# Performance work log

Measured on AMD Instinct MI355X. Metric: run time of the kernel, lower is better.

Reference implementation:

```python
import jax, jax.numpy as jnp
import numpy as np

N_NODES = 20000
N_EDGES = 5000
STEPS = 50
INFECTION_RATE = 0.01
RECOVERY_RATE = 0.038
EDGE_DENSITY = 0.002  # ~10 hyperedges per node on average


def setup_inputs() -> dict:
    key = jax.random.key(0)
    k1, k2 = jax.random.split(key, 2)
    # initial SIR state per node: valid probability rows summing to 1
    u = jax.random.uniform(k1, (N_NODES, 3), dtype=jnp.float32)
    x = u / u.sum(axis=1, keepdims=True)
    # binary hypergraph incidence matrix (num_hyperedges, num_nodes)
    H = (jax.random.uniform(k2, (N_EDGES, N_NODES)) < EDGE_DENSITY).astype(jnp.float32)
    beta = jnp.full((N_NODES,), INFECTION_RATE, dtype=jnp.float32)
    gamma = jnp.full((N_NODES,), RECOVERY_RATE, dtype=jnp.float32)
    return {"x": x, "H": H, "beta": beta, "gamma": gamma, "steps": STEPS}


def reference(x, H, beta, gamma, steps):
    # x: (N, 3) [S, I, R] per node; H: (E, N) incidence.
    def step(state, _):
        S, I, R = state[:, 0], state[:, 1], state[:, 2]
        # hypergraph message passing: node -> hyperedge -> node
        new_cases = beta * (S * (H.T @ (H @ I)))
        new_recovery = gamma * I
        nxt = jnp.stack(
            [S - new_cases, I + new_cases - new_recovery, R + new_recovery], axis=1
        )
        nxt = jnp.maximum(nxt, 0.0)                       # clamp(min=0)
        nxt = nxt / nxt.sum(axis=1, keepdims=True)        # per-node row normalize
        return nxt, nxt

    _, traj = jax.lax.scan(step, x, None, length=steps - 1)
    # output[0] = initial state, then steps-1 simulated updates -> (steps, N, 3)
    return jnp.concatenate([x[None], traj], axis=0)
```

## Files before the change

kernel.cpp:

```cpp
#include <hip/hip_runtime.h>
#include <hip/hip_bf16.h>


#define EDGE_CAP 96
#define NODE_CAP 32

__global__ void zero_counts_kernel(int* edge_cnt, int* node_cnt, int n_edges, int n_nodes) {
    int i = blockIdx.x * blockDim.x + threadIdx.x;
    if (i < n_edges) edge_cnt[i] = 0;
    if (i < n_nodes) node_cnt[i] = 0;
}

__global__ void build_adjacency_kernel(const float* __restrict__ H,
                                       int* __restrict__ edge_cnt,
                                       int* __restrict__ edge_nodes,
                                       int* __restrict__ node_cnt,
                                       int* __restrict__ node_edges,
                                       int n_nodes) {
    const int e = blockIdx.x;
    const float* row = H + (size_t)e * n_nodes;
    const int n4 = n_nodes >> 2;
    const float4* row4 = (const float4*)row;
    for (int c4 = threadIdx.x; c4 < n4; c4 += blockDim.x) {
        float4 v = row4[c4];
        int cbase = c4 << 2;
        if (v.x != 0.0f) {
            int p = atomicAdd(&edge_cnt[e], 1);
            if (p < EDGE_CAP) edge_nodes[e * EDGE_CAP + p] = cbase;
            int q = atomicAdd(&node_cnt[cbase], 1);
            if (q < NODE_CAP) node_edges[cbase * NODE_CAP + q] = e;
        }
        if (v.y != 0.0f) {
            int c = cbase + 1;
            int p = atomicAdd(&edge_cnt[e], 1);
            if (p < EDGE_CAP) edge_nodes[e * EDGE_CAP + p] = c;
            int q = atomicAdd(&node_cnt[c], 1);
            if (q < NODE_CAP) node_edges[c * NODE_CAP + q] = e;
        }
        if (v.z != 0.0f) {
            int c = cbase + 2;
            int p = atomicAdd(&edge_cnt[e], 1);
            if (p < EDGE_CAP) edge_nodes[e * EDGE_CAP + p] = c;
            int q = atomicAdd(&node_cnt[c], 1);
            if (q < NODE_CAP) node_edges[c * NODE_CAP + q] = e;
        }
        if (v.w != 0.0f) {
            int c = cbase + 3;
            int p = atomicAdd(&edge_cnt[e], 1);
            if (p < EDGE_CAP) edge_nodes[e * EDGE_CAP + p] = c;
            int q = atomicAdd(&node_cnt[c], 1);
            if (q < NODE_CAP) node_edges[c * NODE_CAP + q] = e;
        }
    }
    if (threadIdx.x == 0) {
        for (int c = n4 << 2; c < n_nodes; ++c) {
            if (row[c] != 0.0f) {
                int p = atomicAdd(&edge_cnt[e], 1);
                if (p < EDGE_CAP) edge_nodes[e * EDGE_CAP + p] = c;
                int q = atomicAdd(&node_cnt[c], 1);
                if (q < NODE_CAP) node_edges[c * NODE_CAP + q] = e;
            }
        }
    }
}

__global__ void init_state_kernel(const float* __restrict__ x,
                                  float* __restrict__ S, float* __restrict__ I,
                                  float* __restrict__ R, float* __restrict__ out0,
                                  int n_nodes) {
    int n = blockIdx.x * blockDim.x + threadIdx.x;
    if (n >= n_nodes) return;
    float s = x[n * 3 + 0], iv = x[n * 3 + 1], r = x[n * 3 + 2];
    S[n] = s; I[n] = iv; R[n] = r;
    out0[n * 3 + 0] = s; out0[n * 3 + 1] = iv; out0[n * 3 + 2] = r;
}

__global__ void edge_sum_kernel(const int* __restrict__ edge_cnt,
                                const int* __restrict__ edge_nodes,
                                const float* __restrict__ I,
                                float* __restrict__ y, int n_edges) {
    int wavesPerBlock = blockDim.x >> 6;
    int e = blockIdx.x * wavesPerBlock + (threadIdx.x >> 6);
    int lane = threadIdx.x & 63;
    if (e >= n_edges) return;
    int cnt = min(edge_cnt[e], EDGE_CAP);
    float s = 0.0f;
    for (int i = lane; i < cnt; i += 64) s += I[edge_nodes[e * EDGE_CAP + i]];
    #pragma unroll
    for (int off = 32; off > 0; off >>= 1) s += __shfl_down(s, off, 64);
    if (lane == 0) y[e] = s;
}

__global__ void node_update_kernel(const int* __restrict__ node_cnt,
                                   const int* __restrict__ node_edges,
                                   const float* __restrict__ y,
                                   const float* __restrict__ beta,
                                   const float* __restrict__ gamma,
                                   float* __restrict__ S, float* __restrict__ I,
                                   float* __restrict__ R, float* __restrict__ out_t,
                                   int n_nodes) {
    int n = blockIdx.x * blockDim.x + threadIdx.x;
    if (n >= n_nodes) return;
    int cnt = min(node_cnt[n], NODE_CAP);
    float z = 0.0f;
    for (int i = 0; i < cnt; ++i) z += y[node_edges[n * NODE_CAP + i]];
    float s = S[n], iv = I[n], r = R[n];
    float nc = beta[n] * s * z;
    float nr = gamma[n] * iv;
    float s2 = fmaxf(s - nc, 0.0f);
    float i2 = fmaxf(iv + nc - nr, 0.0f);
    float r2 = fmaxf(r + nr, 0.0f);
    float inv = 1.0f / (s2 + i2 + r2);
    s2 *= inv; i2 *= inv; r2 *= inv;
    S[n] = s2; I[n] = i2; R[n] = r2;
    out_t[n * 3 + 0] = s2; out_t[n * 3 + 1] = i2; out_t[n * 3 + 2] = r2;
}

extern "C" void kernel_launch(void* const* d_in, const int* in_sizes, int n_in,
                              void* d_out, int out_size, void* d_ws, size_t ws_size,
                              hipStream_t stream) {
    const float* x     = (const float*)d_in[0];
    const float* H     = (const float*)d_in[1];
    const float* beta  = (const float*)d_in[2];
    const float* gamma = (const float*)d_in[3];
    float* out = (float*)d_out;

    const int n_nodes = in_sizes[0] / 3;
    const int n_edges = in_sizes[1] / n_nodes;
    const int steps   = out_size / in_sizes[0];

    char* ws = (char*)d_ws;
    int*   edge_cnt   = (int*)ws;                         ws += (size_t)n_edges * 4;
    int*   node_cnt   = (int*)ws;                         ws += (size_t)n_nodes * 4;
    int*   edge_nodes = (int*)ws;                         ws += (size_t)n_edges * EDGE_CAP * 4;
    int*   node_edges = (int*)ws;                         ws += (size_t)n_nodes * NODE_CAP * 4;
    float* y          = (float*)ws;                       ws += (size_t)n_edges * 4;
    float* S          = (float*)ws;                       ws += (size_t)n_nodes * 4;
    float* I          = (float*)ws;                       ws += (size_t)n_nodes * 4;
    float* R          = (float*)ws;                       ws += (size_t)n_nodes * 4;

    {
        int mx = max(n_edges, n_nodes);
        zero_counts_kernel<<<(mx + 255) / 256, 256, 0, stream>>>(edge_cnt, node_cnt, n_edges, n_nodes);
    }
    build_adjacency_kernel<<<n_edges, 256, 0, stream>>>(H, edge_cnt, edge_nodes,
                                                        node_cnt, node_edges, n_nodes);
    init_state_kernel<<<(n_nodes + 255) / 256, 256, 0, stream>>>(x, S, I, R, out, n_nodes);

    const int wavesPerBlock = 4;
    const int edgeGrid = (n_edges + wavesPerBlock - 1) / wavesPerBlock;
    for (int t = 1; t < steps; ++t) {
        edge_sum_kernel<<<edgeGrid, 256, 0, stream>>>(edge_cnt, edge_nodes, I, y, n_edges);
        node_update_kernel<<<(n_nodes + 255) / 256, 256, 0, stream>>>(
            node_cnt, node_edges, y, beta, gamma, S, I, R,
            out + (size_t)t * n_nodes * 3, n_nodes);
    }
}
```

Baseline: 1.068 ms.

## Fuse time-step loop into persistent kernel with software grid barrier

Replaces the 98 per-step kernel launches (edge sum and node update) plus the init kernel with a single persistent kernel of 128 blocks by 1024 threads. Steps are separated by an atomic-counter grid barrier, so launch overhead and kernel gaps go away. The edge sum is unrolled to two fixed gathers per lane. The change relies on all 128 blocks being co-resident to avoid deadlock, and each barrier adds atomic spin latency. The H scan is dominated by the 400MB read of H and stays unchanged.

```diff
diff --git a/kernel.cpp b/kernel.cpp
--- a/kernel.cpp
+++ b/kernel.cpp
@@ -5,10 +5,15 @@
 #define EDGE_CAP 96
 #define NODE_CAP 32
 
-__global__ void zero_counts_kernel(int* edge_cnt, int* node_cnt, int n_edges, int n_nodes) {
+#define LOOP_BLOCKS 128
+#define LOOP_THREADS 1024
+
+__global__ void zero_counts_kernel(int* edge_cnt, int* node_cnt, unsigned* bar_ctr,
+                                   int n_edges, int n_nodes) {
     int i = blockIdx.x * blockDim.x + threadIdx.x;
     if (i < n_edges) edge_cnt[i] = 0;
     if (i < n_nodes) node_cnt[i] = 0;
+    if (i == 0) *bar_ctr = 0u;
 }
 
 __global__ void build_adjacency_kernel(const float* __restrict__ H,
@@ -24,32 +29,16 @@
     for (int c4 = threadIdx.x; c4 < n4; c4 += blockDim.x) {
         float4 v = row4[c4];
         int cbase = c4 << 2;
-        if (v.x != 0.0f) {
-            int p = atomicAdd(&edge_cnt[e], 1);
-            if (p < EDGE_CAP) edge_nodes[e * EDGE_CAP + p] = cbase;
-            int q = atomicAdd(&node_cnt[cbase], 1);
-            if (q < NODE_CAP) node_edges[cbase * NODE_CAP + q] = e;
-        }
-        if (v.y != 0.0f) {
-            int c = cbase + 1;
-            int p = atomicAdd(&edge_cnt[e], 1);
-            if (p < EDGE_CAP) edge_nodes[e * EDGE_CAP + p] = c;
-            int q = atomicAdd(&node_cnt[c], 1);
-            if (q < NODE_CAP) node_edges[c * NODE_CAP + q] = e;
-        }
-        if (v.z != 0.0f) {
-            int c = cbase + 2;
-            int p = atomicAdd(&edge_cnt[e], 1);
-            if (p < EDGE_CAP) edge_nodes[e * EDGE_CAP + p] = c;
-            int q = atomicAdd(&node_cnt[c], 1);
-            if (q < NODE_CAP) node_edges[c * NODE_CAP + q] = e;
-        }
-        if (v.w != 0.0f) {
-            int c = cbase + 3;
-            int p = atomicAdd(&edge_cnt[e], 1);
-            if (p < EDGE_CAP) edge_nodes[e * EDGE_CAP + p] = c;
-            int q = atomicAdd(&node_cnt[c], 1);
-            if (q < NODE_CAP) node_edges[c * NODE_CAP + q] = e;
+        float vals[4] = {v.x, v.y, v.z, v.w};
+        #pragma unroll
+        for (int j = 0; j < 4; ++j) {
+            if (vals[j] != 0.0f) {
+                int c = cbase + j;
+                int p = atomicAdd(&edge_cnt[e], 1);
+                if (p < EDGE_CAP) edge_nodes[e * EDGE_CAP + p] = c;
+                int q = atomicAdd(&node_cnt[c], 1);
+                if (q < NODE_CAP) node_edges[c * NODE_CAP + q] = e;
+            }
         }
     }
     if (threadIdx.x == 0) {
@@ -64,56 +53,81 @@
     }
 }
 
-__global__ void init_state_kernel(const float* __restrict__ x,
-                                  float* __restrict__ S, float* __restrict__ I,
-                                  float* __restrict__ R, float* __restrict__ out0,
-                                  int n_nodes) {
-    int n = blockIdx.x * blockDim.x + threadIdx.x;
-    if (n >= n_nodes) return;
-    float s = x[n * 3 + 0], iv = x[n * 3 + 1], r = x[n * 3 + 2];
-    S[n] = s; I[n] = iv; R[n] = r;
-    out0[n * 3 + 0] = s; out0[n * 3 + 1] = iv; out0[n * 3 + 2] = r;
+__device__ __forceinline__ void gsync(unsigned* __restrict__ ctr, unsigned target) {
+    __syncthreads();
+    if (threadIdx.x == 0) {
+        __threadfence();
+        __hip_atomic_fetch_add(ctr, 1u, __ATOMIC_RELEASE, __HIP_MEMORY_SCOPE_AGENT);
+        unsigned v;
+        do {
+            v = __hip_atomic_load(ctr, __ATOMIC_ACQUIRE, __HIP_MEMORY_SCOPE_AGENT);
+            if (v < target) __builtin_amdgcn_s_sleep(2);
+        } while (v < target);
+        __threadfence();
+    }
+    __syncthreads();
 }
 
-__global__ void edge_sum_kernel(const int* __restrict__ edge_cnt,
-                                const int* __restrict__ edge_nodes,
-                                const float* __restrict__ I,
-                                float* __restrict__ y, int n_edges) {
-    int wavesPerBlock = blockDim.x >> 6;
-    int e = blockIdx.x * wavesPerBlock + (threadIdx.x >> 6);
-    int lane = threadIdx.x & 63;
-    if (e >= n_edges) return;
-    int cnt = min(edge_cnt[e], EDGE_CAP);
-    float s = 0.0f;
-    for (int i = lane; i < cnt; i += 64) s += I[edge_nodes[e * EDGE_CAP + i]];
-    #pragma unroll
-    for (int off = 32; off > 0; off >>= 1) s += __shfl_down(s, off, 64);
-    if (lane == 0) y[e] = s;
-}
+__global__ void __launch_bounds__(LOOP_THREADS)
+sir_loop_kernel(const float* __restrict__ x,
+                const float* __restrict__ beta,
+                const float* __restrict__ gamma,
+                const int* __restrict__ edge_cnt,
+                const int* __restrict__ edge_nodes,
+                const int* __restrict__ node_cnt,
+                const int* __restrict__ node_edges,
+                float* __restrict__ y,
+                float* __restrict__ S, float* __restrict__ I, float* __restrict__ R,
+                float* __restrict__ out,
+                int n_nodes, int n_edges, int steps,
+                unsigned* __restrict__ bar_ctr) {
+    const int tid = blockIdx.x * blockDim.x + threadIdx.x;
+    const int nthreads = gridDim.x * blockDim.x;
+    const int wavesPerBlock = blockDim.x >> 6;
+    const int wid = blockIdx.x * wavesPerBlock + (threadIdx.x >> 6);
+    const int nwaves = gridDim.x * wavesPerBlock;
+    const int lane = threadIdx.x & 63;
+    unsigned barnum = 0;
 
-__global__ void node_update_kernel(const int* __restrict__ node_cnt,
-                                   const int* __restrict__ node_edges,
-                                   const float* __restrict__ y,
-                                   const float* __restrict__ beta,
-                                   const float* __restrict__ gamma,
-                                   float* __restrict__ S, float* __restrict__ I,
-                                   float* __restrict__ R, float* __restrict__ out_t,
-                                   int n_nodes) {
-    int n = blockIdx.x * blockDim.x + threadIdx.x;
-    if (n >= n_nodes) return;
-    int cnt = min(node_cnt[n], NODE_CAP);
-    float z = 0.0f;
-    for (int i = 0; i < cnt; ++i) z += y[node_edges[n * NODE_CAP + i]];
-    float s = S[n], iv = I[n], r = R[n];
-    float nc = beta[n] * s * z;
-    float nr = gamma[n] * iv;
-    float s2 = fmaxf(s - nc, 0.0f);
-    float i2 = fmaxf(iv + nc - nr, 0.0f);
-    float r2 = fmaxf(r + nr, 0.0f);
-    float inv = 1.0f / (s2 + i2 + r2);
-    s2 *= inv; i2 *= inv; r2 *= inv;
-    S[n] = s2; I[n] = i2; R[n] = r2;
-    out_t[n * 3 + 0] = s2; out_t[n * 3 + 1] = i2; out_t[n * 3 + 2] = r2;
+    for (int n = tid; n < n_nodes; n += nthreads) {
+        float s = x[n * 3 + 0], iv = x[n * 3 + 1], r = x[n * 3 + 2];
+        S[n] = s; I[n] = iv; R[n] = r;
+        out[n * 3 + 0] = s; out[n * 3 + 1] = iv; out[n * 3 + 2] = r;
+    }
+    gsync(bar_ctr, (++barnum) * gridDim.x);
+
+    for (int t = 1; t < steps; ++t) {
+        for (int e = wid; e < n_edges; e += nwaves) {
+            int cnt = min(edge_cnt[e], EDGE_CAP);
+            const int* idx = edge_nodes + e * EDGE_CAP;
+            float s = 0.0f;
+            if (lane < cnt) s = I[idx[lane]];
+            if (lane + 64 < cnt) s += I[idx[lane + 64]];
+            #pragma unroll
+            for (int off = 32; off > 0; off >>= 1) s += __shfl_down(s, off, 64);
+            if (lane == 0) y[e] = s;
+        }
+        gsync(bar_ctr, (++barnum) * gridDim.x);
+
+        float* out_t = out + (size_t)t * n_nodes * 3;
+        for (int n = tid; n < n_nodes; n += nthreads) {
+            int cnt = min(node_cnt[n], NODE_CAP);
+            const int* eidx = node_edges + n * NODE_CAP;
+            float z = 0.0f;
+            for (int i = 0; i < cnt; ++i) z += y[eidx[i]];
+            float s = S[n], iv = I[n], r = R[n];
+            float nc = beta[n] * s * z;
+            float nr = gamma[n] * iv;
+            float s2 = fmaxf(s - nc, 0.0f);
+            float i2 = fmaxf(iv + nc - nr, 0.0f);
+            float r2 = fmaxf(r + nr, 0.0f);
+            float inv = 1.0f / (s2 + i2 + r2);
+            s2 *= inv; i2 *= inv; r2 *= inv;
+            S[n] = s2; I[n] = i2; R[n] = r2;
+            out_t[n * 3 + 0] = s2; out_t[n * 3 + 1] = i2; out_t[n * 3 + 2] = r2;
+        }
+        gsync(bar_ctr, (++barnum) * gridDim.x);
+    }
 }
 
 extern "C" void kernel_launch(void* const* d_in, const int* in_sizes, int n_in,
@@ -130,6 +144,7 @@
     const int steps   = out_size / in_sizes[0];
 
     char* ws = (char*)d_ws;
+    unsigned* bar_ctr  = (unsigned*)ws;                   ws += 256;
     int*   edge_cnt   = (int*)ws;                         ws += (size_t)n_edges * 4;
     int*   node_cnt   = (int*)ws;                         ws += (size_t)n_nodes * 4;
     int*   edge_nodes = (int*)ws;                         ws += (size_t)n_edges * EDGE_CAP * 4;
@@ -141,18 +156,12 @@
 
     {
         int mx = max(n_edges, n_nodes);
-        zero_counts_kernel<<<(mx + 255) / 256, 256, 0, stream>>>(edge_cnt, node_cnt, n_edges, n_nodes);
+        zero_counts_kernel<<<(mx + 255) / 256, 256, 0, stream>>>(edge_cnt, node_cnt, bar_ctr,
+                                                                 n_edges, n_nodes);
     }
     build_adjacency_kernel<<<n_edges, 256, 0, stream>>>(H, edge_cnt, edge_nodes,
                                                         node_cnt, node_edges, n_nodes);
-    init_state_kernel<<<(n_nodes + 255) / 256, 256, 0, stream>>>(x, S, I, R, out, n_nodes);
-
-    const int wavesPerBlock = 4;
-    const int edgeGrid = (n_edges + wavesPerBlock - 1) / wavesPerBlock;
-    for (int t = 1; t < steps; ++t) {
-        edge_sum_kernel<<<edgeGrid, 256, 0, stream>>>(edge_cnt, edge_nodes, I, y, n_edges);
-        node_update_kernel<<<(n_nodes + 255) / 256, 256, 0, stream>>>(
-            node_cnt, node_edges, y, beta, gamma, S, I, R,
-            out + (size_t)t * n_nodes * 3, n_nodes);
-    }
+    sir_loop_kernel<<<LOOP_BLOCKS, LOOP_THREADS, 0, stream>>>(
+        x, beta, gamma, edge_cnt, edge_nodes, node_cnt, node_edges,
+        y, S, I, R, out, n_nodes, n_edges, steps, bar_ctr);
 }
```

New measurement: 3.987 ms. +273.4%, slower.
